# Kernel optimization log

Measured on AMD Instinct MI355X. Metric: run time of the kernel, lower is better.

Reference implementation:

```python
import jax, jax.numpy as jnp
import numpy as np

NEG_SLOPE = 0.2

def gat_conv(x, src, dst, W, a_src, a_dst, bias, N):
    # PyG GATConv, heads=1: h = xW; e_ij = LeakyReLU(a_src.h_j + a_dst.h_i)
    h = x @ W                                   # [N, H]
    as_ = h @ a_src                             # [N]
    ad_ = h @ a_dst                             # [N]
    e = jax.nn.leaky_relu(as_[src] + ad_[dst], NEG_SLOPE)   # [E]
    m = jax.ops.segment_max(e, dst, num_segments=N)          # per-target max
    w = jnp.exp(e - m[dst])
    denom = jax.ops.segment_sum(w, dst, num_segments=N)
    alpha = w / (denom[dst] + 1e-16)                          # [E]
    out = jax.ops.segment_sum(alpha[:, None] * h[src], dst, num_segments=N)
    return out + bias


def setup_inputs() -> dict:
    key = jax.random.key(0)
    N, E, D, H, A = 20000, 320000, 256, 256, 8
    ks = jax.random.split(key, 16)
    s = lambda k, shp, fan: jax.random.normal(k, shp, jnp.float32) * (1.0 / np.sqrt(fan))
    return {
        "obs": jax.random.normal(ks[0], (N, D), jnp.float32),
        "edge_index": jax.random.randint(ks[1], (2, E), 0, N, dtype=jnp.int32),
        "W1": s(ks[2], (D, H), D), "a1_src": s(ks[3], (H,), H), "a1_dst": s(ks[4], (H,), H), "b1": jnp.zeros((H,), jnp.float32),
        "W2": s(ks[5], (H, H), H), "a2_src": s(ks[6], (H,), H), "a2_dst": s(ks[7], (H,), H), "b2": jnp.zeros((H,), jnp.float32),
        "Wm1": s(ks[8], (H, H), H), "bm1": jnp.zeros((H,), jnp.float32),
        "Wm2": s(ks[9], (H, A), H), "bm2": jnp.zeros((A,), jnp.float32),
    }


def reference(obs, edge_index, W1, a1_src, a1_dst, b1, W2, a2_src, a2_dst, b2, Wm1, bm1, Wm2, bm2):
    N = obs.shape[0]
    loops = jnp.arange(N, dtype=edge_index.dtype)
    src = jnp.concatenate([edge_index[0], loops])   # add self-loops (PyG default)
    dst = jnp.concatenate([edge_index[1], loops])
    x = jax.nn.relu(gat_conv(obs, src, dst, W1, a1_src, a1_dst, b1, N))
    x = jax.nn.relu(gat_conv(x,   src, dst, W2, a2_src, a2_dst, b2, N))
    x = jax.nn.relu(x @ Wm1 + bm1)
    return jnp.tanh(x @ Wm2 + bm2)
```

## Files before the change

### kernel.cpp

```cpp
#include <hip/hip_runtime.h>
#include <hip/hip_bf16.h>
#include <math.h>
#include <stdio.h>

typedef __attribute__((ext_vector_type(8))) short short8;
typedef __attribute__((ext_vector_type(4))) float f32x4;
typedef __attribute__((ext_vector_type(4))) unsigned short us4;
typedef unsigned short us_t;

__device__ __forceinline__ float us2f(unsigned short u) {
    return __uint_as_float(((unsigned)u) << 16);
}
__device__ __forceinline__ unsigned short f2us_rtn(float f) {
    return (unsigned short)__bfloat16_as_ushort(__float2bfloat16(f));
}

__global__ void prep3_wT(const float* __restrict__ Wa, const float* __restrict__ Wb,
                         const float* __restrict__ Wc,
                         unsigned short* __restrict__ HiA, unsigned short* __restrict__ LoA,
                         unsigned short* __restrict__ HiB, unsigned short* __restrict__ LoB,
                         unsigned short* __restrict__ HiC, unsigned short* __restrict__ LoC,
                         int K, int Nn) {
    const int tot = K * Nn;
    int idx = blockIdx.x * blockDim.x + threadIdx.x;
    if (idx >= 3 * tot) return;
    const float* W;
    unsigned short *Hi, *Lo;
    if (idx < tot) { W = Wa; Hi = HiA; Lo = LoA; }
    else if (idx < 2 * tot) { W = Wb; Hi = HiB; Lo = LoB; idx -= tot; }
    else { W = Wc; Hi = HiC; Lo = LoC; idx -= 2 * tot; }
    const int n = idx / K, k = idx - n * K;
    const float f = W[(size_t)k * Nn + n];
    const unsigned u = __float_as_uint(f);
    Hi[idx] = (unsigned short)(u >> 16);
    const float hf = __uint_as_float(u & 0xffff0000u);
    Lo[idx] = (unsigned short)(__float_as_uint(f - hf) >> 16);
}

__global__ void prep_obs(const float* __restrict__ X, unsigned short* __restrict__ Xb, int tot8) {
    const int i = blockIdx.x * blockDim.x + threadIdx.x;
    if (i >= tot8) return;
    const float4 a = *(const float4*)(X + (size_t)i * 8);
    const float4 b = *(const float4*)(X + (size_t)i * 8 + 4);
    short8 o;
    const float f[8] = {a.x, a.y, a.z, a.w, b.x, b.y, b.z, b.w};
#pragma unroll
    for (int e = 0; e < 8; e++) o[e] = (short)f2us_rtn(f[e]);
    *(short8*)(Xb + (size_t)i * 8) = o;
}

#define LP 72
template <bool BIASRELU>
__global__ __launch_bounds__(256) void gemm_mfma(const unsigned short* __restrict__ A,
                                                 const unsigned short* __restrict__ BtHi,
                                                 const unsigned short* __restrict__ BtLo,
                                                 const float* __restrict__ bias,
                                                 unsigned short* __restrict__ C,
                                                 int M, int Nn, int K) {
    __shared__ unsigned short sA[64 * LP];
    __shared__ unsigned short sBh[128 * LP];
    __shared__ unsigned short sBl[128 * LP];
    const int tid = threadIdx.x;
    const int wave = tid >> 6, lane = tid & 63;
    const int m16 = lane & 15, quad = lane >> 4;
    const int row0 = blockIdx.x * 64, col0 = blockIdx.y * 128;
    const int wr = (wave >> 1) * 32, wc = (wave & 1) * 64;
    const int ar = tid >> 2, akc = (tid & 3) * 8;
    const int bkc = (tid & 7) * 8, bcb = tid >> 3;

    f32x4 acc[2][4] = {};
    for (int k0 = 0; k0 < K; k0 += 64) {
        {
            const int gr = (row0 + ar) < M ? (row0 + ar) : (M - 1);
            const unsigned short* Ap = A + (size_t)gr * K + k0 + akc;
            *(short8*)&sA[ar * LP + akc]      = *(const short8*)Ap;
            *(short8*)&sA[ar * LP + akc + 32] = *(const short8*)(Ap + 32);
        }
#pragma unroll
        for (int q = 0; q < 8; q++) {
            const int pl = q >> 2;
            const int colq = bcb + 32 * (q & 3);
            const unsigned short* Bp = (pl ? BtLo : BtHi) + (size_t)(col0 + colq) * K + k0 + bkc;
            unsigned short* sB = pl ? sBl : sBh;
            *(short8*)&sB[colq * LP + bkc] = *(const short8*)Bp;
        }
        __syncthreads();
#pragma unroll
        for (int ks = 0; ks < 2; ks++) {
            short8 ah[2];
#pragma unroll
            for (int mi = 0; mi < 2; mi++)
                ah[mi] = *(const short8*)&sA[(wr + mi * 16 + m16) * LP + ks * 32 + quad * 8];
#pragma unroll
            for (int ni = 0; ni < 4; ni++) {
                const int nb = (wc + ni * 16 + m16) * LP + ks * 32 + quad * 8;
                const short8 bh = *(const short8*)&sBh[nb];
                const short8 bl = *(const short8*)&sBl[nb];
#pragma unroll
                for (int mi = 0; mi < 2; mi++) {
                    acc[mi][ni] = __builtin_amdgcn_mfma_f32_16x16x32_bf16(ah[mi], bh, acc[mi][ni], 0, 0, 0);
                    acc[mi][ni] = __builtin_amdgcn_mfma_f32_16x16x32_bf16(ah[mi], bl, acc[mi][ni], 0, 0, 0);
                }
            }
        }
        __syncthreads();
    }
#pragma unroll
    for (int mi = 0; mi < 2; mi++) {
        const int orow_base = row0 + wr + mi * 16 + quad * 4;
#pragma unroll
        for (int ni = 0; ni < 4; ni++) {
            const int ocol = col0 + wc + ni * 16 + m16;
#pragma unroll
            for (int r = 0; r < 4; r++) {
                const int orow = orow_base + r;
                if (orow < M) {
                    float v = acc[mi][ni][r];
                    if (BIASRELU) { v += bias[ocol]; v = fmaxf(v, 0.f); }
                    C[(size_t)orow * Nn + ocol] = f2us_rtn(v);
                }
            }
        }
    }
}
#undef LP

__global__ __launch_bounds__(256) void dots_kernel(const unsigned short* __restrict__ hb,
                                                   const float* __restrict__ asrc,
                                                   const float* __restrict__ adst,
                                                   float* __restrict__ as_,
                                                   float* __restrict__ ad_, int N) {
    const int wave = threadIdx.x >> 6, lane = threadIdx.x & 63;
    const int n = blockIdx.x * 4 + wave;
    if (n >= N) return;
    const int f = lane * 4;
    const us4 v = *(const us4*)(hb + (size_t)n * 256 + f);
    float s1 = 0.f, s2 = 0.f;
#pragma unroll
    for (int e = 0; e < 4; e++) {
        const float x = us2f(v[e]);
        s1 = fmaf(x, asrc[f + e], s1);
        s2 = fmaf(x, adst[f + e], s2);
    }
#pragma unroll
    for (int off = 32; off; off >>= 1) {
        s1 += __shfl_down(s1, off);
        s2 += __shfl_down(s2, off);
    }
    if (lane == 0) { as_[n] = s1; ad_[n] = s2; }
}

__global__ void init_deg(int* __restrict__ deg, int N) {
    const int i = blockIdx.x * blockDim.x + threadIdx.x;
    if (i < N) deg[i] = 0;
}

__global__ void count_kernel(const int* __restrict__ dstA, int* __restrict__ deg, int E, int Etot) {
    const int e = blockIdx.x * blockDim.x + threadIdx.x;
    if (e >= Etot) return;
    const int d = (e < E) ? dstA[e] : (e - E);
    atomicAdd(&deg[d], 1);
}

__global__ __launch_bounds__(1024) void scan_kernel(const int* __restrict__ deg,
                                                    int* __restrict__ offs,
                                                    int* __restrict__ cursor, int N) {
    __shared__ int sums[1024];
    const int t = threadIdx.x;
    const int chunk = (N + 1023) / 1024;
    const int start = t * chunk;
    int s = 0;
    for (int i = 0; i < chunk; i++) {
        const int p = start + i;
        if (p < N) s += deg[p];
    }
    sums[t] = s;
    __syncthreads();
    for (int off = 1; off < 1024; off <<= 1) {
        const int add = (t >= off) ? sums[t - off] : 0;
        __syncthreads();
        sums[t] += add;
        __syncthreads();
    }
    int run = (t > 0) ? sums[t - 1] : 0;
    for (int i = 0; i < chunk; i++) {
        const int p = start + i;
        if (p < N) { offs[p] = run; cursor[p] = run; run += deg[p]; }
    }
    if (t == 0) offs[N] = sums[1023];
}

__global__ void scatter_kernel(const int* __restrict__ srcA, const int* __restrict__ dstA,
                               int* __restrict__ cursor, int* __restrict__ esrc, int E, int Etot) {
    const int e = blockIdx.x * blockDim.x + threadIdx.x;
    if (e >= Etot) return;
    int s, d;
    if (e < E) { s = srcA[e]; d = dstA[e]; } else { s = d = e - E; }
    const int slot = atomicAdd(&cursor[d], 1);
    esrc[slot] = s;
}

__global__ __launch_bounds__(128) void agg_kernel(const unsigned short* __restrict__ hb,
                                                  const int* __restrict__ offs,
                                                  const int* __restrict__ esrc,
                                                  const float* __restrict__ as_,
                                                  const float* __restrict__ ad_,
                                                  const float* __restrict__ bias,
                                                  unsigned short* __restrict__ xout, int N) {
    const int n = blockIdx.x;
    const int f0 = threadIdx.x * 2;
    const int b = offs[n], e2 = offs[n + 1];
    const float adn = ad_[n];
    float ax = 0.f, ay = 0.f, wsum = 0.f;
    int j = b;
    for (; j + 8 <= e2; j += 8) {
        int s[8];
#pragma unroll
        for (int u = 0; u < 8; u++) s[u] = esrc[j + u];
        unsigned pv[8];
#pragma unroll
        for (int u = 0; u < 8; u++) pv[u] = *(const unsigned*)(hb + (size_t)s[u] * 256 + f0);
        float w[8];
#pragma unroll
        for (int u = 0; u < 8; u++) {
            float v = as_[s[u]] + adn;
            v = v > 0.f ? v : 0.2f * v;
            w[u] = __expf(v);
        }
#pragma unroll
        for (int u = 0; u < 8; u++) {
            ax = fmaf(w[u], us2f((unsigned short)(pv[u] & 0xffffu)), ax);
            ay = fmaf(w[u], us2f((unsigned short)(pv[u] >> 16)), ay);
            wsum += w[u];
        }
    }
    for (; j < e2; j++) {
        const int s = esrc[j];
        float v = as_[s] + adn;
        v = v > 0.f ? v : 0.2f * v;
        const float w = __expf(v);
        const unsigned pv = *(const unsigned*)(hb + (size_t)s * 256 + f0);
        ax = fmaf(w, us2f((unsigned short)(pv & 0xffffu)), ax);
        ay = fmaf(w, us2f((unsigned short)(pv >> 16)), ay);
        wsum += w;
    }
    const float inv = 1.0f / (wsum + 1e-16f);
    float rx = ax * inv + bias[f0];
    float ry = ay * inv + bias[f0 + 1];
    rx = rx > 0.f ? rx : 0.f;
    ry = ry > 0.f ? ry : 0.f;
    const unsigned pack = (unsigned)f2us_rtn(rx) | ((unsigned)f2us_rtn(ry) << 16);
    *(unsigned*)(xout + (size_t)n * 256 + f0) = pack;
}

__global__ __launch_bounds__(256) void final_kernel(const unsigned short* __restrict__ xb,
                                                    const float* __restrict__ W,
                                                    const float* __restrict__ bias,
                                                    float* __restrict__ out, int N, int A) {
    const int wave = threadIdx.x >> 6, lane = threadIdx.x & 63;
    const int n = blockIdx.x * 4 + wave;
    if (n >= N) return;
    const int k0 = lane * 4;
    const us4 v = *(const us4*)(xb + (size_t)n * 256 + k0);
    float p[8] = {};
#pragma unroll
    for (int e = 0; e < 4; e++) {
        const float xv = us2f(v[e]);
#pragma unroll
        for (int a = 0; a < 8; a++) p[a] = fmaf(xv, W[(k0 + e) * A + a], p[a]);
    }
#pragma unroll
    for (int off = 32; off; off >>= 1)
#pragma unroll
        for (int a = 0; a < 8; a++) p[a] += __shfl_down(p[a], off);
    if (lane == 0) {
        for (int a = 0; a < A; a++) out[(size_t)n * A + a] = tanhf(p[a] + bias[a]);
    }
}

__global__ void guard_kernel(const float* __restrict__ out) {
    if (threadIdx.x != 0 || blockIdx.x != 0) return;
    const float o0 = out[0];
    if (fabsf(o0) > 0.f && o0 == o0) return;
    printf("GUARD o0=%e o1=%e\n", (double)o0, (double)out[1]);
}

extern "C" void kernel_launch(void* const* d_in, const int* in_sizes, int n_in,
                              void* d_out, int out_size, void* d_ws, size_t ws_size,
                              hipStream_t stream) {
    const float* obs = (const float*)d_in[0];
    const int* eidx  = (const int*)d_in[1];
    const float* W1  = (const float*)d_in[2];
    const float* a1s = (const float*)d_in[3];
    const float* a1d = (const float*)d_in[4];
    const float* b1  = (const float*)d_in[5];
    const float* W2  = (const float*)d_in[6];
    const float* a2s = (const float*)d_in[7];
    const float* a2d = (const float*)d_in[8];
    const float* b2v = (const float*)d_in[9];
    const float* Wm1 = (const float*)d_in[10];
    const float* bm1 = (const float*)d_in[11];
    const float* Wm2 = (const float*)d_in[12];
    const float* bm2 = (const float*)d_in[13];
    float* out = (float*)d_out;

    const int Hh = in_sizes[3];
    const int Dd = in_sizes[2] / Hh;
    const int N  = in_sizes[0] / Dd;
    const int E  = in_sizes[1] / 2;
    const int Etot = E + N;
    const int Aout = in_sizes[12] / Hh;

    const int* srcA = eidx;
    const int* dstA = eidx + E;

    size_t off = 0;
    char* ws = (char*)d_ws;
    auto alloc = [&](size_t bytes) -> char* {
        char* p = ws + off;
        off = (off + bytes + 15) & ~(size_t)15;
        return p;
    };
    unsigned short* obs_b = (unsigned short*)alloc((size_t)N * Dd * 2);
    unsigned short* h     = (unsigned short*)alloc((size_t)N * Hh * 2);
    unsigned short* xb    = (unsigned short*)alloc((size_t)N * Hh * 2);
    float* as_   = (float*)alloc((size_t)N * 4);
    float* ad_   = (float*)alloc((size_t)N * 4);
    int* deg     = (int*)alloc((size_t)N * 4);
    int* offs    = (int*)alloc((size_t)(N + 1) * 4);
    int* cursor  = (int*)alloc((size_t)N * 4);
    int* esrc    = (int*)alloc((size_t)Etot * 4);
    const size_t wsz = (size_t)Dd * Hh;
    unsigned short* W1tH = (unsigned short*)alloc(wsz * 2);
    unsigned short* W1tL = (unsigned short*)alloc(wsz * 2);
    unsigned short* W2tH = (unsigned short*)alloc(wsz * 2);
    unsigned short* W2tL = (unsigned short*)alloc(wsz * 2);
    unsigned short* WmtH = (unsigned short*)alloc(wsz * 2);
    unsigned short* WmtL = (unsigned short*)alloc(wsz * 2);

    const int eb = 256;
    const int eg = (Etot + eb - 1) / eb;
    const int ng = (N + 255) / 256;
    const dim3 ggrid((N + 63) / 64, Hh / 128);
    const int nb4 = (N + 3) / 4;

    const int p3 = (3 * (int)wsz + 255) / 256;
    prep3_wT<<<p3, 256, 0, stream>>>(W1, W2, Wm1, W1tH, W1tL, W2tH, W2tL, WmtH, WmtL, Dd, Hh);
    const int tot8 = (N * Dd) / 8;
    prep_obs<<<(tot8 + 255) / 256, 256, 0, stream>>>(obs, obs_b, tot8);

    init_deg<<<ng, 256, 0, stream>>>(deg, N);
    count_kernel<<<eg, eb, 0, stream>>>(dstA, deg, E, Etot);
    scan_kernel<<<1, 1024, 0, stream>>>(deg, offs, cursor, N);
    scatter_kernel<<<eg, eb, 0, stream>>>(srcA, dstA, cursor, esrc, E, Etot);

    gemm_mfma<false><<<ggrid, 256, 0, stream>>>(obs_b, W1tH, W1tL, nullptr, h, N, Hh, Dd);
    dots_kernel<<<nb4, 256, 0, stream>>>(h, a1s, a1d, as_, ad_, N);
    agg_kernel<<<N, 128, 0, stream>>>(h, offs, esrc, as_, ad_, b1, xb, N);

    gemm_mfma<false><<<ggrid, 256, 0, stream>>>(xb, W2tH, W2tL, nullptr, h, N, Hh, Hh);
    dots_kernel<<<nb4, 256, 0, stream>>>(h, a2s, a2d, as_, ad_, N);
    agg_kernel<<<N, 128, 0, stream>>>(h, offs, esrc, as_, ad_, b2v, xb, N);

    gemm_mfma<true><<<ggrid, 256, 0, stream>>>(xb, WmtH, WmtL, bm1, h, N, Hh, Hh);
    final_kernel<<<nb4, 256, 0, stream>>>(h, Wm2, bm2, out, N, Aout);

    guard_kernel<<<1, 64, 0, stream>>>(out);
}
```

Before: 302.7 us.

## Drop split-bf16 weight path, fuse attention dots into GEMM epilogue, merge prep kernels

```diff
diff --git a/kernel.cpp b/kernel.cpp
--- a/kernel.cpp
+++ b/kernel.cpp
@@ -6,7 +6,6 @@
 typedef __attribute__((ext_vector_type(8))) short short8;
 typedef __attribute__((ext_vector_type(4))) float f32x4;
 typedef __attribute__((ext_vector_type(4))) unsigned short us4;
-typedef unsigned short us_t;
 
 __device__ __forceinline__ float us2f(unsigned short u) {
     return __uint_as_float(((unsigned)u) << 16);
@@ -15,51 +14,66 @@
     return (unsigned short)__bfloat16_as_ushort(__float2bfloat16(f));
 }
 
-__global__ void prep3_wT(const float* __restrict__ Wa, const float* __restrict__ Wb,
+__global__ void prep_all(const float* __restrict__ Wa, const float* __restrict__ Wb,
                          const float* __restrict__ Wc,
                          unsigned short* __restrict__ HiA, unsigned short* __restrict__ LoA,
                          unsigned short* __restrict__ HiB, unsigned short* __restrict__ LoB,
                          unsigned short* __restrict__ HiC, unsigned short* __restrict__ LoC,
-                         int K, int Nn) {
+                         const float* __restrict__ X, unsigned short* __restrict__ Xb,
+                         float* __restrict__ as1, float* __restrict__ ad1,
+                         float* __restrict__ as2, float* __restrict__ ad2,
+                         int* __restrict__ deg,
+                         int K, int Nn, int N, int tot8) {
     const int tot = K * Nn;
     int idx = blockIdx.x * blockDim.x + threadIdx.x;
-    if (idx >= 3 * tot) return;
-    const float* W;
-    unsigned short *Hi, *Lo;
-    if (idx < tot) { W = Wa; Hi = HiA; Lo = LoA; }
-    else if (idx < 2 * tot) { W = Wb; Hi = HiB; Lo = LoB; idx -= tot; }
-    else { W = Wc; Hi = HiC; Lo = LoC; idx -= 2 * tot; }
-    const int n = idx / K, k = idx - n * K;
-    const float f = W[(size_t)k * Nn + n];
-    const unsigned u = __float_as_uint(f);
-    Hi[idx] = (unsigned short)(u >> 16);
-    const float hf = __uint_as_float(u & 0xffff0000u);
-    Lo[idx] = (unsigned short)(__float_as_uint(f - hf) >> 16);
-}
-
-__global__ void prep_obs(const float* __restrict__ X, unsigned short* __restrict__ Xb, int tot8) {
-    const int i = blockIdx.x * blockDim.x + threadIdx.x;
-    if (i >= tot8) return;
-    const float4 a = *(const float4*)(X + (size_t)i * 8);
-    const float4 b = *(const float4*)(X + (size_t)i * 8 + 4);
-    short8 o;
-    const float f[8] = {a.x, a.y, a.z, a.w, b.x, b.y, b.z, b.w};
-#pragma unroll
-    for (int e = 0; e < 8; e++) o[e] = (short)f2us_rtn(f[e]);
-    *(short8*)(Xb + (size_t)i * 8) = o;
+    if (idx < 3 * tot) {
+        const float* W;
+        unsigned short *Hi, *Lo;
+        if (idx < tot) { W = Wa; Hi = HiA; Lo = LoA; }
+        else if (idx < 2 * tot) { W = Wb; Hi = HiB; Lo = LoB; idx -= tot; }
+        else { W = Wc; Hi = HiC; Lo = LoC; idx -= 2 * tot; }
+        const int n = idx / K, k = idx - n * K;
+        const float f = W[(size_t)k * Nn + n];
+        const unsigned u = __float_as_uint(f);
+        Hi[idx] = (unsigned short)(u >> 16);
+        const float hf = __uint_as_float(u & 0xffff0000u);
+        Lo[idx] = (unsigned short)(__float_as_uint(f - hf) >> 16);
+        return;
+    }
+    idx -= 3 * tot;
+    if (idx < 5 * N) {
+        if (idx < N) as1[idx] = 0.f;
+        else if (idx < 2 * N) ad1[idx - N] = 0.f;
+        else if (idx < 3 * N) as2[idx - 2 * N] = 0.f;
+        else if (idx < 4 * N) ad2[idx - 3 * N] = 0.f;
+        else deg[idx - 4 * N] = 0;
+        return;
+    }
+    idx -= 5 * N;
+    if (idx < tot8) {
+        const float4 a = *(const float4*)(X + (size_t)idx * 8);
+        const float4 b = *(const float4*)(X + (size_t)idx * 8 + 4);
+        short8 o;
+        const float f[8] = {a.x, a.y, a.z, a.w, b.x, b.y, b.z, b.w};
+#pragma unroll
+        for (int e = 0; e < 8; e++) o[e] = (short)f2us_rtn(f[e]);
+        *(short8*)(Xb + (size_t)idx * 8) = o;
+    }
 }
 
 #define LP 72
-template <bool BIASRELU>
+template <bool BIASRELU, bool DOTS>
 __global__ __launch_bounds__(256) void gemm_mfma(const unsigned short* __restrict__ A,
-                                                 const unsigned short* __restrict__ BtHi,
-                                                 const unsigned short* __restrict__ BtLo,
+                                                 const unsigned short* __restrict__ Bt,
                                                  const float* __restrict__ bias,
+                                                 const float* __restrict__ avs,
+                                                 const float* __restrict__ avd,
+                                                 float* __restrict__ as_,
+                                                 float* __restrict__ ad_,
                                                  unsigned short* __restrict__ C,
                                                  int M, int Nn, int K) {
     __shared__ unsigned short sA[64 * LP];
-    __shared__ unsigned short sBh[128 * LP];
-    __shared__ unsigned short sBl[128 * LP];
+    __shared__ unsigned short sB[128 * LP];
     const int tid = threadIdx.x;
     const int wave = tid >> 6, lane = tid & 63;
     const int m16 = lane & 15, quad = lane >> 4;
@@ -77,12 +91,10 @@
             *(short8*)&sA[ar * LP + akc + 32] = *(const short8*)(Ap + 32);
         }
 #pragma unroll
-        for (int q = 0; q < 8; q++) {
-            const int pl = q >> 2;
-            const int colq = bcb + 32 * (q & 3);
-            const unsigned short* Bp = (pl ? BtLo : BtHi) + (size_t)(col0 + colq) * K + k0 + bkc;
-            unsigned short* sB = pl ? sBl : sBh;
-            *(short8*)&sB[colq * LP + bkc] = *(const short8*)Bp;
+        for (int q = 0; q < 4; q++) {
+            const int colq = bcb + 32 * q;
+            *(short8*)&sB[colq * LP + bkc] =
+                *(const short8*)(Bt + (size_t)(col0 + colq) * K + k0 + bkc);
         }
         __syncthreads();
 #pragma unroll
@@ -93,24 +105,23 @@
                 ah[mi] = *(const short8*)&sA[(wr + mi * 16 + m16) * LP + ks * 32 + quad * 8];
 #pragma unroll
             for (int ni = 0; ni < 4; ni++) {
-                const int nb = (wc + ni * 16 + m16) * LP + ks * 32 + quad * 8;
-                const short8 bh = *(const short8*)&sBh[nb];
-                const short8 bl = *(const short8*)&sBl[nb];
-#pragma unroll
-                for (int mi = 0; mi < 2; mi++) {
-                    acc[mi][ni] = __builtin_amdgcn_mfma_f32_16x16x32_bf16(ah[mi], bh, acc[mi][ni], 0, 0, 0);
-                    acc[mi][ni] = __builtin_amdgcn_mfma_f32_16x16x32_bf16(ah[mi], bl, acc[mi][ni], 0, 0, 0);
-                }
+                const short8 bv = *(const short8*)&sB[(wc + ni * 16 + m16) * LP + ks * 32 + quad * 8];
+#pragma unroll
+                for (int mi = 0; mi < 2; mi++)
+                    acc[mi][ni] = __builtin_amdgcn_mfma_f32_16x16x32_bf16(ah[mi], bv, acc[mi][ni], 0, 0, 0);
             }
         }
         __syncthreads();
     }
+    float ps[2][4] = {}, pd[2][4] = {};
 #pragma unroll
     for (int mi = 0; mi < 2; mi++) {
         const int orow_base = row0 + wr + mi * 16 + quad * 4;
 #pragma unroll
         for (int ni = 0; ni < 4; ni++) {
             const int ocol = col0 + wc + ni * 16 + m16;
+            float asv = 0.f, adv = 0.f;
+            if (DOTS) { asv = avs[ocol]; adv = avd[ocol]; }
 #pragma unroll
             for (int r = 0; r < 4; r++) {
                 const int orow = orow_base + r;
@@ -118,42 +129,39 @@
                     float v = acc[mi][ni][r];
                     if (BIASRELU) { v += bias[ocol]; v = fmaxf(v, 0.f); }
                     C[(size_t)orow * Nn + ocol] = f2us_rtn(v);
+                    if (DOTS) { ps[mi][r] = fmaf(v, asv, ps[mi][r]); pd[mi][r] = fmaf(v, adv, pd[mi][r]); }
                 }
             }
         }
     }
+    if (DOTS) {
+#pragma unroll
+        for (int mi = 0; mi < 2; mi++)
+#pragma unroll
+            for (int r = 0; r < 4; r++) {
+#pragma unroll
+                for (int off = 1; off < 16; off <<= 1) {
+                    ps[mi][r] += __shfl_xor(ps[mi][r], off);
+                    pd[mi][r] += __shfl_xor(pd[mi][r], off);
+                }
+            }
+        if (m16 == 0) {
+#pragma unroll
+            for (int mi = 0; mi < 2; mi++) {
+                const int orow_base = row0 + wr + mi * 16 + quad * 4;
+#pragma unroll
+                for (int r = 0; r < 4; r++) {
+                    const int orow = orow_base + r;
+                    if (orow < M) {
+                        atomicAdd(&as_[orow], ps[mi][r]);
+                        atomicAdd(&ad_[orow], pd[mi][r]);
+                    }
+                }
+            }
+        }
+    }
 }
 #undef LP
-
-__global__ __launch_bounds__(256) void dots_kernel(const unsigned short* __restrict__ hb,
-                                                   const float* __restrict__ asrc,
-                                                   const float* __restrict__ adst,
-                                                   float* __restrict__ as_,
-                                                   float* __restrict__ ad_, int N) {
-    const int wave = threadIdx.x >> 6, lane = threadIdx.x & 63;
-    const int n = blockIdx.x * 4 + wave;
-    if (n >= N) return;
-    const int f = lane * 4;
-    const us4 v = *(const us4*)(hb + (size_t)n * 256 + f);
-    float s1 = 0.f, s2 = 0.f;
-#pragma unroll
-    for (int e = 0; e < 4; e++) {
-        const float x = us2f(v[e]);
-        s1 = fmaf(x, asrc[f + e], s1);
-        s2 = fmaf(x, adst[f + e], s2);
-    }
-#pragma unroll
-    for (int off = 32; off; off >>= 1) {
-        s1 += __shfl_down(s1, off);
-        s2 += __shfl_down(s2, off);
-    }
-    if (lane == 0) { as_[n] = s1; ad_[n] = s2; }
-}
-
-__global__ void init_deg(int* __restrict__ deg, int N) {
-    const int i = blockIdx.x * blockDim.x + threadIdx.x;
-    if (i < N) deg[i] = 0;
-}
 
 __global__ void count_kernel(const int* __restrict__ dstA, int* __restrict__ deg, int E, int Etot) {
     const int e = blockIdx.x * blockDim.x + threadIdx.x;
@@ -324,8 +332,10 @@
     unsigned short* obs_b = (unsigned short*)alloc((size_t)N * Dd * 2);
     unsigned short* h     = (unsigned short*)alloc((size_t)N * Hh * 2);
     unsigned short* xb    = (unsigned short*)alloc((size_t)N * Hh * 2);
-    float* as_   = (float*)alloc((size_t)N * 4);
-    float* ad_   = (float*)alloc((size_t)N * 4);
+    float* as1   = (float*)alloc((size_t)N * 4);
+    float* ad1   = (float*)alloc((size_t)N * 4);
+    float* as2   = (float*)alloc((size_t)N * 4);
+    float* ad2   = (float*)alloc((size_t)N * 4);
     int* deg     = (int*)alloc((size_t)N * 4);
     int* offs    = (int*)alloc((size_t)(N + 1) * 4);
     int* cursor  = (int*)alloc((size_t)N * 4);
@@ -340,29 +350,29 @@
 
     const int eb = 256;
     const int eg = (Etot + eb - 1) / eb;
-    const int ng = (N + 255) / 256;
     const dim3 ggrid((N + 63) / 64, Hh / 128);
     const int nb4 = (N + 3) / 4;
 
-    const int p3 = (3 * (int)wsz + 255) / 256;
-    prep3_wT<<<p3, 256, 0, stream>>>(W1, W2, Wm1, W1tH, W1tL, W2tH, W2tL, WmtH, WmtL, Dd, Hh);
     const int tot8 = (N * Dd) / 8;
-    prep_obs<<<(tot8 + 255) / 256, 256, 0, stream>>>(obs, obs_b, tot8);
-
-    init_deg<<<ng, 256, 0, stream>>>(deg, N);
+    const int ptot = 3 * (int)wsz + 5 * N + tot8;
+    prep_all<<<(ptot + 255) / 256, 256, 0, stream>>>(
+        W1, W2, Wm1, W1tH, W1tL, W2tH, W2tL, WmtH, WmtL,
+        obs, obs_b, as1, ad1, as2, ad2, deg, Dd, Hh, N, tot8);
+
     count_kernel<<<eg, eb, 0, stream>>>(dstA, deg, E, Etot);
     scan_kernel<<<1, 1024, 0, stream>>>(deg, offs, cursor, N);
     scatter_kernel<<<eg, eb, 0, stream>>>(srcA, dstA, cursor, esrc, E, Etot);
 
-    gemm_mfma<false><<<ggrid, 256, 0, stream>>>(obs_b, W1tH, W1tL, nullptr, h, N, Hh, Dd);
-    dots_kernel<<<nb4, 256, 0, stream>>>(h, a1s, a1d, as_, ad_, N);
-    agg_kernel<<<N, 128, 0, stream>>>(h, offs, esrc, as_, ad_, b1, xb, N);
-
-    gemm_mfma<false><<<ggrid, 256, 0, stream>>>(xb, W2tH, W2tL, nullptr, h, N, Hh, Hh);
-    dots_kernel<<<nb4, 256, 0, stream>>>(h, a2s, a2d, as_, ad_, N);
-    agg_kernel<<<N, 128, 0, stream>>>(h, offs, esrc, as_, ad_, b2v, xb, N);
-
-    gemm_mfma<true><<<ggrid, 256, 0, stream>>>(xb, WmtH, WmtL, bm1, h, N, Hh, Hh);
+    gemm_mfma<false, true><<<ggrid, 256, 0, stream>>>(obs_b, W1tH, nullptr, a1s, a1d,
+                                                      as1, ad1, h, N, Hh, Dd);
+    agg_kernel<<<N, 128, 0, stream>>>(h, offs, esrc, as1, ad1, b1, xb, N);
+
+    gemm_mfma<false, true><<<ggrid, 256, 0, stream>>>(xb, W2tH, nullptr, a2s, a2d,
+                                                      as2, ad2, h, N, Hh, Hh);
+    agg_kernel<<<N, 128, 0, stream>>>(h, offs, esrc, as2, ad2, b2v, xb, N);
+
+    gemm_mfma<true, false><<<ggrid, 256, 0, stream>>>(xb, WmtH, bm1, nullptr, nullptr,
+                                                      nullptr, nullptr, h, N, Hh, Hh);
     final_kernel<<<nb4, 256, 0, stream>>>(h, Wm2, bm2, out, N, Aout);
 
     guard_kernel<<<1, 64, 0, stream>>>(out);
```

After: 284.6 us. -6.0%, faster.
